# Kernel optimization log

Measured on AMD Instinct MI355X. Metric: run time of the kernel, lower is better.

The kernel has to match this reference:

```python
import math
import jax, jax.numpy as jnp
import numpy as np

EPS = 1e-6
MAX_SCALE_LOG = math.log(100.0)

def rms_norm(x, scale, eps=EPS):
    # x * scale / rms(x), reduction over last dim
    ms = jnp.mean(jnp.square(x), axis=-1, keepdims=True)
    return x * (scale * jax.lax.rsqrt(ms + eps))

def axial_rope_theta(pos, n_heads, d_head, dtype):
    # freqs: linspace in log-space from pi to 10*pi, reshaped to [n_heads, d_head//4]
    f = np.exp(np.linspace(math.log(math.pi), math.log(10.0 * math.pi),
                           n_heads * d_head // 4 + 1)[:-1])
    freqs = jnp.asarray(f.reshape(d_head // 4, n_heads).T, dtype)  # [h, e/4]
    theta_h = pos[:, :, None, 0:1] * freqs  # [n, l, h, e/4]
    theta_w = pos[:, :, None, 1:2] * freqs  # [n, l, h, e/4]
    theta = jnp.concatenate([theta_h, theta_w], axis=-1)  # [n, l, h, e/2]
    return theta.transpose(0, 2, 1, 3)  # [n, h, l, e/2]

def apply_rotary(x, theta):
    d = theta.shape[-1]
    x1, x2, x3 = x[..., :d], x[..., d:2 * d], x[..., 2 * d:]
    cos, sin = jnp.cos(theta), jnp.sin(theta)
    return jnp.concatenate([x1 * cos - x2 * sin, x2 * cos + x1 * sin, x3], axis=-1)

def setup_inputs() -> dict:
    key = jax.random.key(0)
    ks = jax.random.split(key, 8)
    n, l, d_model, d_head = 2, 2048, 1024, 64
    n_heads = d_model // d_head
    x = jax.random.normal(ks[0], (n, l, d_model), jnp.float32)
    pos = jax.random.uniform(ks[1], (n, l, 2), jnp.float32)
    cond = jax.random.normal(ks[2], (n, 1, d_model), jnp.float32)
    # params (torch uses zero-init for w_cond/w_out; small random for a non-degenerate baseline)
    w_cond = jax.random.normal(ks[3], (d_model, d_model), jnp.float32) * 0.02
    w_qkv = jax.random.normal(ks[4], (d_model, 3 * d_model), jnp.float32) * (d_model ** -0.5)
    qk_scale = jnp.full((n_heads,), math.log(10.0), jnp.float32)
    w_out = jax.random.normal(ks[5], (d_model, d_model), jnp.float32) * 0.02
    return {"x": x, "pos": pos, "cond": cond, "w_cond": w_cond,
            "w_qkv": w_qkv, "qk_scale": qk_scale, "w_out": w_out}

def reference(x, pos, cond, w_cond, w_qkv, qk_scale, w_out):
    n, l, d_model = x.shape
    h = qk_scale.shape[0]
    e = d_model // h
    # AdaRMSNorm: scale = linear(cond) + 1
    xn = rms_norm(x, cond @ w_cond + 1.0)
    # QKV projection
    q, k, v = jnp.split(xn @ w_qkv, 3, axis=-1)
    to_heads = lambda t: t.reshape(n, l, h, e).transpose(0, 2, 1, 3)  # [n,h,l,e]
    q, k, v = to_heads(q), to_heads(k), to_heads(v)
    # QKNorm: per-head learned scale, rms over head dim
    s = jnp.exp(0.5 * jnp.minimum(qk_scale, MAX_SCALE_LOG) - 0.25 * math.log(e))
    q = rms_norm(q, s[:, None, None])
    k = rms_norm(k, s[:, None, None])
    # Axial RoPE
    theta = axial_rope_theta(pos, h, e, x.dtype)
    q = apply_rotary(q, theta)
    k = apply_rotary(k, theta)
    # SDPA (no mask)
    attn = jax.nn.softmax(jnp.einsum('nhqe,nhke->nhqk', q, k) / math.sqrt(e), axis=-1)
    o = jnp.einsum('nhqk,nhke->nhqe', attn, v)
    o = o.transpose(0, 2, 1, 3).reshape(n, l, d_model)
    return o @ w_out
```

## Files before the change

### kernel.cpp

```cpp
#include <hip/hip_runtime.h>

typedef unsigned short u16;
typedef unsigned int u32;
typedef short s16x8 __attribute__((ext_vector_type(8)));
typedef short s16x4 __attribute__((ext_vector_type(4)));
typedef float f32x4 __attribute__((ext_vector_type(4)));
typedef u32 u32x2 __attribute__((ext_vector_type(2)));

#define AS1 __attribute__((address_space(1)))
#define AS3 __attribute__((address_space(3)))

__device__ __forceinline__ float bf2f(u16 u) {
    union { unsigned int i; float f; } x; x.i = ((unsigned int)u) << 16; return x.f;
}
__device__ __forceinline__ u16 f2bf(float f) {
    union { float f; unsigned int i; } x; x.f = f;
    unsigned int r = (x.i + 0x7FFFu + ((x.i >> 16) & 1u)) >> 16;
    return (u16)r;
}
__device__ __forceinline__ void storeOut(u16* p, float v) { *p = f2bf(v); }
__device__ __forceinline__ void storeOut(float* p, float v) { *p = v; }
__device__ __forceinline__ float loadIn(const void* p, size_t i, int isf32) {
    return isf32 ? ((const float*)p)[i] : bf2f(((const u16*)p)[i]);
}
__device__ __forceinline__ float fexp2(float x) {
#if __has_builtin(__builtin_amdgcn_exp2f)
    return __builtin_amdgcn_exp2f(x);
#else
    return exp2f(x);
#endif
}
__device__ __forceinline__ u32 pack_bf(float a, float b) {
    u32 ua = __float_as_uint(a) + 0x8000u;
    u32 ub = __float_as_uint(b) + 0x8000u;
    return __builtin_amdgcn_perm(ub, ua, 0x07060302u);
}

__global__ __launch_bounds__(256) void detect_dtype(const u16* __restrict__ x,
                                                    int* __restrict__ flag) {
    __shared__ int cnt[4];
    const int tid = threadIdx.x;
    int c = 0;
    #pragma unroll
    for (int i = 0; i < 4; ++i) {
        const u16 u = x[tid * 4 + i];
        const int e = (u >> 7) & 0xFF;
        c += (e >= 101 && e <= 135) ? 1 : 0;
    }
    #pragma unroll
    for (int m = 1; m < 64; m <<= 1) c += __shfl_xor(c, m, 64);
    if ((tid & 63) == 0) cnt[tid >> 6] = c;
    __syncthreads();
    if (tid == 0) {
        const int t = cnt[0] + cnt[1] + cnt[2] + cnt[3];
        *flag = (t < 800) ? 1 : 0;
    }
}

__global__ __launch_bounds__(256) void cond_gemv(const void* __restrict__ cond,
                                                 const void* __restrict__ w,
                                                 float* __restrict__ out,
                                                 const int* __restrict__ flag) {
    const int isf32 = *flag;
    const int d  = blockIdx.x * 256 + threadIdx.x;
    const int n  = blockIdx.y;
    const int k0 = blockIdx.z * 64;
    float acc = 0.f;
    #pragma unroll 8
    for (int k = 0; k < 64; ++k)
        acc += loadIn(cond, n * 1024 + k0 + k, isf32) *
               loadIn(w, (size_t)(k0 + k) * 1024 + d, isf32);
    atomicAdd(out + n * 1024 + d, acc);
}

__global__ __launch_bounds__(256) void rmsnorm_x(const void* __restrict__ x,
                                                 const float* __restrict__ scl,
                                                 u16* __restrict__ xn,
                                                 const int* __restrict__ flag) {
    const int isf32 = *flag;
    const int tok = blockIdx.x;
    const int n = tok >> 11;
    u16* orow = xn + (size_t)tok * 1024;
    const int base = threadIdx.x * 4;
    float f0, f1, f2, f3;
    if (isf32) {
        const float4 v = *(const float4*)((const float*)x + (size_t)tok * 1024 + base);
        f0 = v.x; f1 = v.y; f2 = v.z; f3 = v.w;
    } else {
        s16x4 uv = *(const s16x4*)((const u16*)x + (size_t)tok * 1024 + base);
        f0 = bf2f((u16)uv[0]); f1 = bf2f((u16)uv[1]); f2 = bf2f((u16)uv[2]); f3 = bf2f((u16)uv[3]);
    }
    float ss = f0 * f0 + f1 * f1 + f2 * f2 + f3 * f3;
    #pragma unroll
    for (int m = 1; m < 64; m <<= 1) ss += __shfl_xor(ss, m, 64);
    __shared__ float red[4];
    const int wave = threadIdx.x >> 6, lane = threadIdx.x & 63;
    if (lane == 0) red[wave] = ss;
    __syncthreads();
    float ms = (red[0] + red[1] + red[2] + red[3]) * (1.f / 1024.f);
    float rinv = rsqrtf(ms + 1e-6f);
    orow[base + 0] = f2bf(f0 * (scl[n * 1024 + base + 0] + 1.f) * rinv);
    orow[base + 1] = f2bf(f1 * (scl[n * 1024 + base + 1] + 1.f) * rinv);
    orow[base + 2] = f2bf(f2 * (scl[n * 1024 + base + 2] + 1.f) * rinv);
    orow[base + 3] = f2bf(f3 * (scl[n * 1024 + base + 3] + 1.f) * rinv);
}

__global__ __launch_bounds__(256) void transpose_bf(const void* __restrict__ src,
                                                    u16* __restrict__ dst, int R, int C,
                                                    const int* __restrict__ flag) {
    const int isf32 = *flag;
    __shared__ u16 t[32][33];
    const int c0 = blockIdx.x * 32, r0 = blockIdx.y * 32;
    const int tx = threadIdx.x & 31, ty = threadIdx.x >> 5;
    #pragma unroll
    for (int i = 0; i < 4; ++i)
        t[ty + i * 8][tx] = f2bf(loadIn(src, (size_t)(r0 + ty + i * 8) * C + c0 + tx, isf32));
    __syncthreads();
    #pragma unroll
    for (int i = 0; i < 4; ++i)
        dst[(size_t)(c0 + ty + i * 8) * R + r0 + tx] = t[tx][ty + i * 8];
}

__global__ __launch_bounds__(256) void transpose_v(const u16* __restrict__ qkv,
                                                   u16* __restrict__ vtg) {
    __shared__ u16 t[64][65];
    const int nh = blockIdx.y, l0 = blockIdx.x * 64;
    const int n = nh >> 4, h = nh & 15;
    const int tid = threadIdx.x;
    const u16* src = qkv + (size_t)(n * 2048 + l0) * 3072 + 2048 + h * 64;
    #pragma unroll
    for (int it = 0; it < 16; ++it) {
        const int idx = it * 256 + tid;
        const int row = idx >> 6, col = idx & 63;
        t[row][col] = src[(size_t)row * 3072 + col];
    }
    __syncthreads();
    u16* dst = vtg + (size_t)nh * 64 * 2048 + l0;
    #pragma unroll
    for (int it = 0; it < 16; ++it) {
        const int idx = it * 256 + tid;
        const int er = idx >> 6, lc = idx & 63;
        dst[(size_t)er * 2048 + lc] = t[lc][er];
    }
}

template <typename OutT>
__global__ __launch_bounds__(256) void gemm_bt(const u16* __restrict__ A,
                                               const u16* __restrict__ BT,
                                               OutT* __restrict__ C, int Nn, int K) {
    __shared__ u16 As[128 * 32];
    __shared__ u16 Bs[128 * 32];
    const int tid = threadIdx.x;
    const int wave = tid >> 6, lane = tid & 63;
    const int l15 = lane & 15, quad = lane >> 4;
    const int bm0 = blockIdx.y * 128, bn0 = blockIdx.x * 128;
    const int wr = wave >> 1, wc = wave & 1;
    f32x4 acc[4][4] = {};
    const int srow = lane >> 2;
    const int g = (lane & 3) ^ (srow & 3);
    for (int bk = 0; bk < K; bk += 32) {
        __syncthreads();
        #pragma unroll
        for (int p = 0; p < 2; ++p) {
            const int rowl = p * 64 + wave * 16 + srow;
            const u16* ga = A + (size_t)(bm0 + rowl) * K + bk + g * 8;
            u16* la = As + (p * 64 + wave * 16) * 32;
            __builtin_amdgcn_global_load_lds((const AS1 void*)ga, (AS3 void*)la, 16, 0, 0);
            const u16* gb = BT + (size_t)(bn0 + rowl) * K + bk + g * 8;
            u16* lb = Bs + (p * 64 + wave * 16) * 32;
            __builtin_amdgcn_global_load_lds((const AS1 void*)gb, (AS3 void*)lb, 16, 0, 0);
        }
        __syncthreads();
        s16x8 af[4], bfr[4];
        #pragma unroll
        for (int mt = 0; mt < 4; ++mt) {
            const int r = wr * 64 + mt * 16 + l15;
            af[mt] = *(const s16x8*)(As + r * 32 + ((quad ^ (r & 3)) << 3));
        }
        #pragma unroll
        for (int nt = 0; nt < 4; ++nt) {
            const int r = wc * 64 + nt * 16 + l15;
            bfr[nt] = *(const s16x8*)(Bs + r * 32 + ((quad ^ (r & 3)) << 3));
        }
        #pragma unroll
        for (int mt = 0; mt < 4; ++mt)
            #pragma unroll
            for (int nt = 0; nt < 4; ++nt)
                acc[mt][nt] = __builtin_amdgcn_mfma_f32_16x16x32_bf16(af[mt], bfr[nt], acc[mt][nt], 0, 0, 0);
    }
    #pragma unroll
    for (int mt = 0; mt < 4; ++mt)
        #pragma unroll
        for (int nt = 0; nt < 4; ++nt)
            #pragma unroll
            for (int r = 0; r < 4; ++r) {
                const int row = bm0 + wr * 64 + mt * 16 + quad * 4 + r;
                const int col = bn0 + wc * 64 + nt * 16 + l15;
                storeOut(C + (size_t)row * Nn + col, acc[mt][nt][r]);
            }
}

__global__ __launch_bounds__(256) void qk_head(const u16* __restrict__ qkv,
                                               const void* __restrict__ pos,
                                               const void* __restrict__ qk_scale,
                                               u16* __restrict__ q_ws,
                                               u16* __restrict__ k_ws,
                                               const int* __restrict__ flag) {
    const int isf32 = *flag;
    const int gw = blockIdx.x * 4 + (threadIdx.x >> 6);
    const int lane = threadIdx.x & 63;
    const int tok = gw >> 4, h = gw & 15;
    const int n = tok >> 11, l = tok & 2047;
    const u16* row = qkv + (size_t)tok * 3072;
    float qv = bf2f(row[h * 64 + lane]);
    float kv = bf2f(row[1024 + h * 64 + lane]);
    float q2 = qv * qv, k2 = kv * kv;
    #pragma unroll
    for (int m = 1; m < 64; m <<= 1) { q2 += __shfl_xor(q2, m, 64); k2 += __shfl_xor(k2, m, 64); }
    float qn = qv * rsqrtf(q2 * (1.f / 64.f) + 1e-6f);
    float kn = kv * rsqrtf(k2 * (1.f / 64.f) + 1e-6f);
    const float qs = loadIn(qk_scale, h, isf32);
    const float s = __expf(0.5f * fminf(qs, 4.605170186f) - 1.039720771f);
    qn *= s * s * 0.125f * 1.44269504089f;
    const int j = lane & 31;
    const float p = loadIn(pos, tok * 2 + (j >> 4), isf32);
    const float t = (float)((j & 15) * 16 + h);
    const float freq = 3.14159265358979f * __expf(t * (2.302585093f / 256.f));
    const float th = p * freq;
    const float c = __cosf(th), sn = __sinf(th);
    const float pq = __shfl_xor(qn, 32, 64);
    const float pk = __shfl_xor(kn, 32, 64);
    float qr, kr;
    if (lane < 32) { qr = qn * c - pq * sn; kr = kn * c - pk * sn; }
    else           { qr = qn * c + pq * sn; kr = kn * c + pk * sn; }
    const size_t oidx = ((size_t)(n * 16 + h) * 2048 + l) * 64 + lane;
    q_ws[oidx] = f2bf(qr);
    k_ws[oidx] = f2bf(kr);
}

__global__ __launch_bounds__(256, 2) void attn3(const u16* __restrict__ Q,
                                                const u16* __restrict__ K,
                                                const u16* __restrict__ Vtg,
                                                u16* __restrict__ O) {
    __shared__ u16 Ks[128 * 64];
    __shared__ u16 Vt[64 * 128];
    __shared__ u16 Ps[4 * 32 * 136];
    const int nh = blockIdx.y;
    const int q0 = blockIdx.x * 128;
    const int tid = threadIdx.x;
    const int wave = tid >> 6, lane = tid & 63;
    const int l15 = lane & 15, quad = lane >> 4;
    const size_t hb = (size_t)nh * 2048 * 64;

    s16x8 qf[2][2];
    #pragma unroll
    for (int qg = 0; qg < 2; ++qg)
        #pragma unroll
        for (int kc = 0; kc < 2; ++kc)
            qf[qg][kc] = *(const s16x8*)(Q + hb + (size_t)(q0 + wave * 32 + qg * 16 + l15) * 64 + kc * 32 + quad * 8);

    f32x4 Oacc[2][4] = {};
    float lacc[2] = {0.f, 0.f};
    u16* Pw = Ps + wave * (32 * 136);

    for (int kb = 0; kb < 2048; kb += 128) {
        __syncthreads();
        {
            const int r8 = lane >> 3, c8 = lane & 7;
            #pragma unroll
            for (int p = 0; p < 4; ++p) {
                const int rloc = wave * 32 + p * 8 + r8;
                const int d = c8 ^ (rloc & 7);
                __builtin_amdgcn_global_load_lds(
                    (const AS1 void*)(K + hb + (size_t)(kb + rloc) * 64 + d * 8),
                    (AS3 void*)(Ks + (wave * 32 + p * 8) * 64), 16, 0, 0);
            }
        }
        {
            const int r4 = lane >> 4, c16 = lane & 15;
            #pragma unroll
            for (int p = 0; p < 4; ++p) {
                const int e = wave * 16 + p * 4 + r4;
                const int d = c16 ^ (e & 7);
                __builtin_amdgcn_global_load_lds(
                    (const AS1 void*)(Vtg + (size_t)nh * 64 * 2048 + (size_t)e * 2048 + kb + d * 8),
                    (AS3 void*)(Vt + (wave * 16 + p * 4) * 128), 16, 0, 0);
            }
        }
        __syncthreads();

        f32x4 S[2][8] = {};
        #pragma unroll
        for (int kt = 0; kt < 8; ++kt) {
            const int r = kt * 16 + l15;
            #pragma unroll
            for (int kc = 0; kc < 2; ++kc) {
                const s16x8 kf = *(const s16x8*)(Ks + r * 64 + (((kc * 4 + quad) ^ (r & 7)) << 3));
                S[0][kt] = __builtin_amdgcn_mfma_f32_16x16x32_bf16(kf, qf[0][kc], S[0][kt], 0, 0, 0);
                S[1][kt] = __builtin_amdgcn_mfma_f32_16x16x32_bf16(kf, qf[1][kc], S[1][kt], 0, 0, 0);
            }
        }

        #pragma unroll
        for (int qg = 0; qg < 2; ++qg) {
            float rs = 0.f;
            #pragma unroll
            for (int kt = 0; kt < 8; ++kt) {
                const float e0 = fexp2(S[qg][kt][0] - 15.f);
                const float e1 = fexp2(S[qg][kt][1] - 15.f);
                const float e2 = fexp2(S[qg][kt][2] - 15.f);
                const float e3 = fexp2(S[qg][kt][3] - 15.f);
                rs += (e0 + e1) + (e2 + e3);
                u32x2 pk2;
                pk2[0] = pack_bf(e0, e1);
                pk2[1] = pack_bf(e2, e3);
                *(u32x2*)(Pw + (qg * 16 + l15) * 136 + kt * 16 + quad * 4) = pk2;
            }
            lacc[qg] += rs;
        }

        #pragma unroll
        for (int kc = 0; kc < 4; ++kc) {
            const s16x8 pf0 = *(const s16x8*)(Pw + l15 * 136 + kc * 32 + quad * 8);
            const s16x8 pf1 = *(const s16x8*)(Pw + (16 + l15) * 136 + kc * 32 + quad * 8);
            #pragma unroll
            for (int nto = 0; nto < 4; ++nto) {
                const int e = nto * 16 + l15;
                const s16x8 vf = *(const s16x8*)(Vt + e * 128 + (((kc * 4 + quad) ^ (e & 7)) << 3));
                Oacc[0][nto] = __builtin_amdgcn_mfma_f32_16x16x32_bf16(pf0, vf, Oacc[0][nto], 0, 0, 0);
                Oacc[1][nto] = __builtin_amdgcn_mfma_f32_16x16x32_bf16(pf1, vf, Oacc[1][nto], 0, 0, 0);
            }
        }
    }

    #pragma unroll
    for (int qg = 0; qg < 2; ++qg) {
        lacc[qg] += __shfl_xor(lacc[qg], 16, 64);
        lacc[qg] += __shfl_xor(lacc[qg], 32, 64);
    }

    const int n = nh >> 4, h = nh & 15;
    #pragma unroll
    for (int qg = 0; qg < 2; ++qg)
        #pragma unroll
        for (int r = 0; r < 4; ++r) {
            const float linv = 1.f / __shfl(lacc[qg], quad * 4 + r, 64);
            const int qrow = q0 + wave * 32 + qg * 16 + quad * 4 + r;
            #pragma unroll
            for (int nto = 0; nto < 4; ++nto)
                O[((size_t)n * 2048 + qrow) * 1024 + h * 64 + nto * 16 + l15] = f2bf(Oacc[qg][nto][r] * linv);
        }
}

extern "C" void kernel_launch(void* const* d_in, const int* in_sizes, int n_in,
                              void* d_out, int out_size, void* d_ws, size_t ws_size,
                              hipStream_t stream) {
    const void* x        = d_in[0];
    const void* pos      = d_in[1];
    const void* cond     = d_in[2];
    const void* w_cond   = d_in[3];
    const void* w_qkv    = d_in[4];
    const void* qk_scale = d_in[5];
    const void* w_out    = d_in[6];

    char* ws = (char*)d_ws;
    constexpr size_t OFS_SCALE = 0;
    constexpr size_t OFS_FLAG  = 8192;
    constexpr size_t OFS_XN    = 16384;
    constexpr size_t OFS_WQKVT = OFS_XN    + 8388608;
    constexpr size_t OFS_WOUTT = OFS_WQKVT + 6291456;
    constexpr size_t OFS_QKV   = OFS_WOUTT + 2097152;
    constexpr size_t OFS_Q     = OFS_QKV   + 25165824;
    constexpr size_t OFS_K     = OFS_Q     + 8388608;
    constexpr size_t OFS_VT    = OFS_K     + 8388608;
    constexpr size_t OFS_O     = OFS_VT    + 8388608;

    float* scale = (float*)(ws + OFS_SCALE);
    int*   flag  = (int*)(ws + OFS_FLAG);
    u16* xn    = (u16*)(ws + OFS_XN);
    u16* wqkvT = (u16*)(ws + OFS_WQKVT);
    u16* woutT = (u16*)(ws + OFS_WOUTT);
    u16* qkv   = (u16*)(ws + OFS_QKV);
    u16* qws   = (u16*)(ws + OFS_Q);
    u16* kws   = (u16*)(ws + OFS_K);
    u16* vtg   = (u16*)(ws + OFS_VT);
    u16* ows   = (u16*)(ws + OFS_O);

    detect_dtype<<<dim3(1), 256, 0, stream>>>((const u16*)x, flag);
    hipMemsetAsync(scale, 0, 2 * 1024 * sizeof(float), stream);
    cond_gemv<<<dim3(4, 2, 16), 256, 0, stream>>>(cond, w_cond, scale, flag);
    rmsnorm_x<<<dim3(4096), 256, 0, stream>>>(x, scale, xn, flag);
    transpose_bf<<<dim3(96, 32), 256, 0, stream>>>(w_qkv, wqkvT, 1024, 3072, flag);
    transpose_bf<<<dim3(32, 32), 256, 0, stream>>>(w_out, woutT, 1024, 1024, flag);
    gemm_bt<u16><<<dim3(24, 32), 256, 0, stream>>>(xn, wqkvT, qkv, 3072, 1024);
    qk_head<<<dim3(16384), 256, 0, stream>>>(qkv, pos, qk_scale, qws, kws, flag);
    transpose_v<<<dim3(32, 32), 256, 0, stream>>>(qkv, vtg);
    attn3<<<dim3(16, 32), 256, 0, stream>>>(qws, kws, vtg, ows);
    gemm_bt<float><<<dim3(8, 32), 256, 0, stream>>>(ows, woutT, (float*)d_out, 1024, 1024);
}
```

Baseline: 245.4 us.

## Double-buffer K/V tiles in attention with 64-key blocks and async prefetch

```diff
diff --git a/kernel.cpp b/kernel.cpp
--- a/kernel.cpp
+++ b/kernel.cpp
@@ -238,19 +238,23 @@
     k_ws[oidx] = f2bf(kr);
 }
 
-__global__ __launch_bounds__(256, 2) void attn3(const u16* __restrict__ Q,
+__global__ __launch_bounds__(256, 2) void attn4(const u16* __restrict__ Q,
                                                 const u16* __restrict__ K,
                                                 const u16* __restrict__ Vtg,
                                                 u16* __restrict__ O) {
-    __shared__ u16 Ks[128 * 64];
-    __shared__ u16 Vt[64 * 128];
-    __shared__ u16 Ps[4 * 32 * 136];
+    __shared__ u16 Ks[2][64 * 64];
+    __shared__ u16 Vt[2][64 * 64];
+    __shared__ u16 Ps[4][32 * 72];
     const int nh = blockIdx.y;
     const int q0 = blockIdx.x * 128;
     const int tid = threadIdx.x;
     const int wave = tid >> 6, lane = tid & 63;
     const int l15 = lane & 15, quad = lane >> 4;
     const size_t hb = (size_t)nh * 2048 * 64;
+    const u16* Vbase = Vtg + (size_t)nh * 64 * 2048;
+
+    const int dr0 = tid >> 3;
+    const int dd  = tid & 7;
 
     s16x8 qf[2][2];
     #pragma unroll
@@ -261,41 +265,47 @@
 
     f32x4 Oacc[2][4] = {};
     float lacc[2] = {0.f, 0.f};
-    u16* Pw = Ps + wave * (32 * 136);
-
-    for (int kb = 0; kb < 2048; kb += 128) {
-        __syncthreads();
-        {
-            const int r8 = lane >> 3, c8 = lane & 7;
-            #pragma unroll
-            for (int p = 0; p < 4; ++p) {
-                const int rloc = wave * 32 + p * 8 + r8;
-                const int d = c8 ^ (rloc & 7);
+    u16* Pw = Ps[wave];
+
+    #pragma unroll
+    for (int it = 0; it < 2; ++it) {
+        const int row = it * 32 + dr0;
+        const int g = dd ^ (row & 7);
+        __builtin_amdgcn_global_load_lds(
+            (const AS1 void*)(K + hb + (size_t)row * 64 + g * 8),
+            (AS3 void*)(Ks[0] + (it * 256 + wave * 64) * 8), 16, 0, 0);
+        __builtin_amdgcn_global_load_lds(
+            (const AS1 void*)(Vbase + (size_t)row * 2048 + g * 8),
+            (AS3 void*)(Vt[0] + (it * 256 + wave * 64) * 8), 16, 0, 0);
+    }
+    __syncthreads();
+
+    for (int i = 0; i < 32; ++i) {
+        const int cur = i & 1;
+        const int kb = i * 64;
+        if (i < 31) {
+            const int nxt = cur ^ 1;
+            const int kbn = kb + 64;
+            #pragma unroll
+            for (int it = 0; it < 2; ++it) {
+                const int row = it * 32 + dr0;
+                const int g = dd ^ (row & 7);
                 __builtin_amdgcn_global_load_lds(
-                    (const AS1 void*)(K + hb + (size_t)(kb + rloc) * 64 + d * 8),
-                    (AS3 void*)(Ks + (wave * 32 + p * 8) * 64), 16, 0, 0);
+                    (const AS1 void*)(K + hb + (size_t)(kbn + row) * 64 + g * 8),
+                    (AS3 void*)(Ks[nxt] + (it * 256 + wave * 64) * 8), 16, 0, 0);
+                __builtin_amdgcn_global_load_lds(
+                    (const AS1 void*)(Vbase + (size_t)row * 2048 + kbn + g * 8),
+                    (AS3 void*)(Vt[nxt] + (it * 256 + wave * 64) * 8), 16, 0, 0);
             }
         }
-        {
-            const int r4 = lane >> 4, c16 = lane & 15;
-            #pragma unroll
-            for (int p = 0; p < 4; ++p) {
-                const int e = wave * 16 + p * 4 + r4;
-                const int d = c16 ^ (e & 7);
-                __builtin_amdgcn_global_load_lds(
-                    (const AS1 void*)(Vtg + (size_t)nh * 64 * 2048 + (size_t)e * 2048 + kb + d * 8),
-                    (AS3 void*)(Vt + (wave * 16 + p * 4) * 128), 16, 0, 0);
-            }
-        }
-        __syncthreads();
-
-        f32x4 S[2][8] = {};
-        #pragma unroll
-        for (int kt = 0; kt < 8; ++kt) {
+
+        f32x4 S[2][4] = {};
+        #pragma unroll
+        for (int kt = 0; kt < 4; ++kt) {
             const int r = kt * 16 + l15;
             #pragma unroll
             for (int kc = 0; kc < 2; ++kc) {
-                const s16x8 kf = *(const s16x8*)(Ks + r * 64 + (((kc * 4 + quad) ^ (r & 7)) << 3));
+                const s16x8 kf = *(const s16x8*)(Ks[cur] + r * 64 + (((kc * 4 + quad) ^ (r & 7)) << 3));
                 S[0][kt] = __builtin_amdgcn_mfma_f32_16x16x32_bf16(kf, qf[0][kc], S[0][kt], 0, 0, 0);
                 S[1][kt] = __builtin_amdgcn_mfma_f32_16x16x32_bf16(kf, qf[1][kc], S[1][kt], 0, 0, 0);
             }
@@ -305,7 +315,7 @@
         for (int qg = 0; qg < 2; ++qg) {
             float rs = 0.f;
             #pragma unroll
-            for (int kt = 0; kt < 8; ++kt) {
+            for (int kt = 0; kt < 4; ++kt) {
                 const float e0 = fexp2(S[qg][kt][0] - 15.f);
                 const float e1 = fexp2(S[qg][kt][1] - 15.f);
                 const float e2 = fexp2(S[qg][kt][2] - 15.f);
@@ -314,23 +324,25 @@
                 u32x2 pk2;
                 pk2[0] = pack_bf(e0, e1);
                 pk2[1] = pack_bf(e2, e3);
-                *(u32x2*)(Pw + (qg * 16 + l15) * 136 + kt * 16 + quad * 4) = pk2;
+                *(u32x2*)(Pw + (qg * 16 + l15) * 72 + kt * 16 + quad * 4) = pk2;
             }
             lacc[qg] += rs;
         }
 
         #pragma unroll
-        for (int kc = 0; kc < 4; ++kc) {
-            const s16x8 pf0 = *(const s16x8*)(Pw + l15 * 136 + kc * 32 + quad * 8);
-            const s16x8 pf1 = *(const s16x8*)(Pw + (16 + l15) * 136 + kc * 32 + quad * 8);
+        for (int kc = 0; kc < 2; ++kc) {
+            const s16x8 pf0 = *(const s16x8*)(Pw + l15 * 72 + kc * 32 + quad * 8);
+            const s16x8 pf1 = *(const s16x8*)(Pw + (16 + l15) * 72 + kc * 32 + quad * 8);
             #pragma unroll
             for (int nto = 0; nto < 4; ++nto) {
                 const int e = nto * 16 + l15;
-                const s16x8 vf = *(const s16x8*)(Vt + e * 128 + (((kc * 4 + quad) ^ (e & 7)) << 3));
+                const s16x8 vf = *(const s16x8*)(Vt[cur] + e * 64 + (((kc * 4 + quad) ^ (e & 7)) << 3));
                 Oacc[0][nto] = __builtin_amdgcn_mfma_f32_16x16x32_bf16(pf0, vf, Oacc[0][nto], 0, 0, 0);
                 Oacc[1][nto] = __builtin_amdgcn_mfma_f32_16x16x32_bf16(pf1, vf, Oacc[1][nto], 0, 0, 0);
             }
         }
+
+        if (i < 31) __syncthreads();
     }
 
     #pragma unroll
@@ -395,6 +407,6 @@
     gemm_bt<u16><<<dim3(24, 32), 256, 0, stream>>>(xn, wqkvT, qkv, 3072, 1024);
     qk_head<<<dim3(16384), 256, 0, stream>>>(qkv, pos, qk_scale, qws, kws, flag);
     transpose_v<<<dim3(32, 32), 256, 0, stream>>>(qkv, vtg);
-    attn3<<<dim3(16, 32), 256, 0, stream>>>(qws, kws, vtg, ows);
+    attn4<<<dim3(16, 32), 256, 0, stream>>>(qws, kws, vtg, ows);
     gemm_bt<float><<<dim3(8, 32), 256, 0, stream>>>(ows, woutT, (float*)d_out, 1024, 1024);
 }
```

New measurement: 244.6 us. No clear change (-0.3%).
